# Kernel tuning notes

Hardware: AMD Instinct MI355X
Metric: run time of the kernel (lower is better)

The kernel has to match this reference:

```python
import jax, jax.numpy as jnp
import numpy as np

W = 64          # word_embedding_size
ES = 64         # entity_embedding_size
H = 4           # head_num
DH = W // H
K = 3           # convolution_num
NW, NQ, NE, NR = 50000, 20000, 200000, 100000
LQ, LR, EP, B = 8, 16, 500000, 1024
D = ES + W      # propagated entity feature dim


def _mhsa_mean(x, Wq, bq, Wk, bk, Wv, bv, Wo, bo):
    # x: [N, L, W] -> [N, W]; standard multi-head self-attention then mean over L
    N, L, _ = x.shape
    q = (x @ Wq + bq).reshape(N, L, H, DH)
    k = (x @ Wk + bk).reshape(N, L, H, DH)
    v = (x @ Wv + bv).reshape(N, L, H, DH)
    s = jnp.einsum('nlhd,nmhd->nhlm', q, k) / jnp.sqrt(jnp.asarray(DH, x.dtype))
    a = jax.nn.softmax(s, axis=-1)
    o = jnp.einsum('nhlm,nmhd->nlhd', a, v).reshape(N, L, W)
    return (o @ Wo + bo).mean(axis=1)


def setup_inputs() -> dict:
    key = jax.random.key(0)
    ks = jax.random.split(key, 20)
    f = jnp.float32
    inp = {
        'word_emb': jax.random.normal(ks[0], (NW, W), f) * 0.02,
        'entity_emb': jax.random.normal(ks[1], (NE, ES), f) * 0.02,
        'Wq': jax.random.normal(ks[2], (W, W), f) * (1.0 / np.sqrt(W)),
        'bq': jnp.zeros((W,), f),
        'Wk': jax.random.normal(ks[3], (W, W), f) * (1.0 / np.sqrt(W)),
        'bk': jnp.zeros((W,), f),
        'Wv': jax.random.normal(ks[4], (W, W), f) * (1.0 / np.sqrt(W)),
        'bv': jnp.zeros((W,), f),
        'Wo': jax.random.normal(ks[5], (W, W), f) * (1.0 / np.sqrt(W)),
        'bo': jnp.zeros((W,), f),
        'review_words': jax.random.randint(ks[6], (NR, LR), 0, NW),
        'query_words_graph': jax.random.randint(ks[7], (NQ, LQ), 0, NW),
        'profile_dst': jax.random.randint(ks[8], (NR,), 0, NE),
        'pur_src': jax.random.randint(ks[9], (EP,), 0, NE),
        'pur_dst': jax.random.randint(ks[10], (EP,), 0, NE),
        'pur_qid': jax.random.randint(ks[11], (EP,), 0, NQ),
        'users': jax.random.randint(ks[12], (B,), 0, NE),
        'items': jax.random.randint(ks[13], (B,), 0, NE),
        'negs': jax.random.randint(ks[14], (B,), 0, NE),
        'query_words': jax.random.randint(ks[15], (B, LQ), 0, NW),
    }
    return inp


def reference(word_emb, entity_emb, Wq, bq, Wk, bk, Wv, bv, Wo, bo,
              review_words, query_words_graph, profile_dst,
              pur_src, pur_dst, pur_qid, users, items, negs, query_words):
    seg = jax.ops.segment_sum
    attn = lambda x: _mhsa_mean(x, Wq, bq, Wk, bk, Wv, bv, Wo, bo)
    we = word_emb.at[0].set(0.0)  # padding_idx=0

    # composes: word -> review / query (mailbox attention reduce)
    rev_h = attn(we[review_words])              # [NR, W]
    q_h = attn(we[query_words_graph])           # [NQ, W]
    q_e0 = jnp.concatenate([jnp.zeros((NQ, ES), we.dtype), q_h], axis=-1)  # [NQ, D]

    # profiles: review -> entity, mean by in-degree
    deg_p = jnp.clip(seg(jnp.ones((NR,), we.dtype), profile_dst, num_segments=NE), 1.0)[:, None]
    prof = seg(rev_h, profile_dst, num_segments=NE) / deg_p   # [NE, W]
    e = jnp.concatenate([entity_emb, prof], axis=-1)          # e_0: [NE, D]

    # deg_i = out_deg(purchased) + out_deg(purchased_by), clamped
    ones_e = jnp.ones((EP,), we.dtype)
    deg_i = jnp.clip(seg(ones_e, pur_src, num_segments=NE)
                     + seg(ones_e, pur_dst, num_segments=NE), 1.0)[:, None]
    inv = 1.0 / jnp.sqrt(deg_i)                               # [NE, 1]

    es = [e]
    for _ in range(K):
        msg = e * inv                                         # e_k / sqrt(deg_i)
        m_pur = e[pur_src] + q_e0[pur_qid] * inv[pur_src]     # msg_u_i UDF
        nxt = seg(m_pur, pur_dst, num_segments=NE) \
            + seg(msg[pur_dst], pur_src, num_segments=NE)     # purchased_by (reverse)
        e = nxt * inv
        es.append(e)
    efin = sum(es) / (K + 1)                                  # [NE, D]

    # batch scoring
    u = efin[users]
    qb = attn(we[query_words])                                # [B, W]
    p = u + jnp.concatenate([jnp.zeros((B, ES), we.dtype), qb], axis=-1)
    pos = jnp.sum(p * efin[items], axis=-1)
    neg = jnp.sum(p * efin[negs], axis=-1)
    loss = -jnp.mean(jax.nn.log_sigmoid(pos - neg))           # BPR loss
    return loss
```

## Files before the change

kernel.cpp:

```cpp
#include <hip/hip_runtime.h>
#include <hip/hip_fp8.h>
#include <cstdint>

#define CDIV(a,b) (((a)+(b)-1)/(b))

typedef __attribute__((ext_vector_type(8))) short bf16x8;
typedef __attribute__((ext_vector_type(4))) float f32x4;
typedef __attribute__((ext_vector_type(8))) float f32x8;
typedef __attribute__((ext_vector_type(4))) _Float16 half4;
typedef __attribute__((ext_vector_type(8))) _Float16 half8;

#define QK_SCALE 32.0f
#define SCORE_SCALE (0.25f / (QK_SCALE * QK_SCALE))
#define EXP2_C (SCORE_SCALE * 1.44269504089f)

#define ES_SCALE 64.0f

__device__ __forceinline__ float bf2f(short s) {
    return __builtin_bit_cast(float, ((unsigned)(unsigned short)s) << 16);
}
__device__ __forceinline__ short rtne(float f) {
    const unsigned u = __builtin_bit_cast(unsigned, f);
    return (short)((u + 0x7fffu + ((u >> 16) & 1u)) >> 16);
}
__device__ __forceinline__ unsigned pack2r(float lo, float hi) {
    return (unsigned)(unsigned short)rtne(lo) | ((unsigned)(unsigned short)rtne(hi) << 16);
}
__device__ __forceinline__ float fp8tof(unsigned char b) {
    __hip_fp8_e4m3 t; t.__x = b; return (float)t;
}
__device__ __forceinline__ unsigned char ftofp8(float f) {
    __hip_fp8_e4m3 t(f); return t.__x;
}
__device__ __forceinline__ f32x8 fp8x8tof32(long v) {
    union { long l; unsigned char b[8]; } u; u.l = v;
    f32x8 r;
    #pragma unroll
    for (int j = 0; j < 8; ++j) r[j] = fp8tof(u.b[j]);
    return r;
}
__device__ __forceinline__ long f32x8tofp8(f32x8 a) {
    union { long l; unsigned char b[8]; } u;
    #pragma unroll
    for (int j = 0; j < 8; ++j) u.b[j] = ftofp8(a[j]);
    return u.l;
}

template<int CTRL>
__device__ __forceinline__ float dpp_add(float x) {
    const int t = __builtin_amdgcn_update_dpp(0, __builtin_bit_cast(int, x),
                                              CTRL, 0xf, 0xf, true);
    return x + __builtin_bit_cast(float, t);
}
__device__ __forceinline__ float rowsum16(float x) {
    x = dpp_add<0x108>(x);
    x = dpp_add<0x104>(x);
    x = dpp_add<0x102>(x);
    x = dpp_add<0x101>(x);
    return x;
}


__device__ __forceinline__ void prep_body(int bid,
    const float* __restrict__ we, const short* __restrict__ Wt,
    const float* __restrict__ bq, const float* __restrict__ bk,
    const float* __restrict__ bv, unsigned char* __restrict__ WQKV, int NW)
{
    const int wave = threadIdx.x >> 6;
    const int lane = threadIdx.x & 63;
    const int quad = lane >> 4;
    const int lm   = lane & 15;
    const int ntiles = CDIV(NW, 16);

    bf16x8 bfr[3][4][2];
    #pragma unroll
    for (int p = 0; p < 3; ++p)
        #pragma unroll
        for (int nt = 0; nt < 4; ++nt)
            #pragma unroll
            for (int kh = 0; kh < 2; ++kh)
                bfr[p][nt][kh] = *(const bf16x8*)(Wt + ((p*64 + nt*16 + lm)*64) + kh*32 + quad*8);
    float bias[3][4];
    #pragma unroll
    for (int nt = 0; nt < 4; ++nt) {
        bias[0][nt] = bq[nt*16 + lm];
        bias[1][nt] = bk[nt*16 + lm];
        bias[2][nt] = bv[nt*16 + lm];
    }

    #pragma unroll
    for (int t = 0; t < 4; ++t) {
        const int tile = (bid*4 + wave)*4 + t;
        if (tile >= ntiles) return;
        const int wb = tile*16;
        int w = wb + lm;
        if (w >= NW) w = NW - 1;
        const float* xr = we + (size_t)w*64;
        union { unsigned u[4]; bf16x8 v; } a0, a1;
        const float4 f0 = *(const float4*)(xr + quad*8);
        const float4 f1 = *(const float4*)(xr + quad*8 + 4);
        const float4 f2 = *(const float4*)(xr + 32 + quad*8);
        const float4 f3 = *(const float4*)(xr + 32 + quad*8 + 4);
        a0.u[0] = pack2r(f0.x, f0.y); a0.u[1] = pack2r(f0.z, f0.w);
        a0.u[2] = pack2r(f1.x, f1.y); a0.u[3] = pack2r(f1.z, f1.w);
        a1.u[0] = pack2r(f2.x, f2.y); a1.u[1] = pack2r(f2.z, f2.w);
        a1.u[2] = pack2r(f3.x, f3.y); a1.u[3] = pack2r(f3.z, f3.w);
        if (w == 0) {
            a0.u[0]=0u; a0.u[1]=0u; a0.u[2]=0u; a0.u[3]=0u;
            a1.u[0]=0u; a1.u[1]=0u; a1.u[2]=0u; a1.u[3]=0u;
        }
        #pragma unroll
        for (int p = 0; p < 3; ++p) {
            #pragma unroll
            for (int nt = 0; nt < 4; ++nt) {
                f32x4 c = {bias[p][nt], bias[p][nt], bias[p][nt], bias[p][nt]};
                c = __builtin_amdgcn_mfma_f32_16x16x32_bf16(a0.v, bfr[p][nt][0], c, 0, 0, 0);
                c = __builtin_amdgcn_mfma_f32_16x16x32_bf16(a1.v, bfr[p][nt][1], c, 0, 0, 0);
                #pragma unroll
                for (int r = 0; r < 4; ++r) {
                    const int w2 = wb + quad*4 + r;
                    if (w2 < NW) {
                        unsigned char* rowo = WQKV + (size_t)w2*192;
                        const int base = (p == 2) ? 128 : (p == 0) ? 64 : 0;
                        rowo[base + nt*16 + lm] = ftofp8(c[r] * QK_SCALE);
                    }
                }
            }
        }
    }
}

__device__ __forceinline__ void fill_body(int bid,
    const int* __restrict__ src, const int* __restrict__ dst,
    const int* __restrict__ qid,
    int* __restrict__ curC, int2* __restrict__ cmb2, int EP)
{
    const int t = bid*256 + threadIdx.x;
    if (t >= EP) return;
    const int s = src[t], d = dst[t];
    const int p1 = atomicAdd(&curC[d], 1);
    int2 e1; e1.x = s; e1.y = qid[t];
    cmb2[p1] = e1;
    const int p2 = atomicAdd(&curC[s], 1);
    int2 e2; e2.x = d | (int)0x80000000; e2.y = 0;
    cmb2[p2] = e2;
}

__device__ __forceinline__ void mark_body(int bid,
    const int* __restrict__ users, const int* __restrict__ items,
    const int* __restrict__ negs, int B, unsigned* __restrict__ lev,
    int* __restrict__ listS, int* __restrict__ list2, int* __restrict__ list1,
    int* __restrict__ nS, int* __restrict__ n2, int* __restrict__ n1)
{
    const int t = bid*256 + threadIdx.x;
    if (t >= 3*B) return;
    const int which = t / B, b = t - which*B;
    const int v = (which == 0) ? users[b] : (which == 1) ? items[b] : negs[b];
    const unsigned old = atomicMax(&lev[v], 3u);
    if (old < 3u) {
        listS[atomicAdd(nS, 1)] = v;
        list2[atomicAdd(n2, 1)] = v;
        list1[atomicAdd(n1, 1)] = v;
    }
}

__device__ __forceinline__ void expand_body(int bid, int nb, unsigned targ,
    const int* __restrict__ slist, const int* __restrict__ pn,
    const int* __restrict__ offC, const int* __restrict__ endC,
    const int2* __restrict__ cmb2, unsigned* __restrict__ lev,
    int* __restrict__ dl1, int* __restrict__ dn1,
    int* __restrict__ dl2, int* __restrict__ dn2)
{
    const int n = *pn;
    const int stride = nb * 256;
    for (int t = bid*256 + threadIdx.x; t < n; t += stride) {
        const int v = slist[t];
        const int b0 = offC[v], e0 = endC[v];
        for (int i = b0; i < e0; ++i) {
            const int u = cmb2[i].x & 0x7fffffff;
            const unsigned old = atomicMax(&lev[u], targ);
            if (old < targ) {
                dl1[atomicAdd(dn1, 1)] = u;
                if (dl2) dl2[atomicAdd(dn2, 1)] = u;
            }
        }
    }
}

__device__ __forceinline__ void finalize_body(int bid,
    const float* __restrict__ emb, const float* __restrict__ prof,
    unsigned char* __restrict__ e8, float* __restrict__ inv,
    const unsigned* __restrict__ deg_p, const unsigned* __restrict__ cntC, int NE)
{
    const int t = bid*256 + threadIdx.x;
    const int v = t >> 5;
    if (v >= NE) return;
    const int c = (t & 31) * 4;
    float4 ev;
    if (c < 64) {
        ev = *(const float4*)&emb[(size_t)v*64 + c];
    } else {
        ev = *(const float4*)&prof[(size_t)v*64 + (c - 64)];
        const unsigned dp = deg_p[v];
        const float r = 1.0f / (float)(dp > 1u ? dp : 1u);
        ev.x *= r; ev.y *= r; ev.z *= r; ev.w *= r;
    }
    union { unsigned u; unsigned char b[4]; } pk;
    pk.b[0] = ftofp8(ev.x * ES_SCALE);
    pk.b[1] = ftofp8(ev.y * ES_SCALE);
    pk.b[2] = ftofp8(ev.z * ES_SCALE);
    pk.b[3] = ftofp8(ev.w * ES_SCALE);
    *(unsigned*)&e8[(size_t)v*128 + c] = pk.u;
    if (c == 0) {
        const unsigned di = cntC[v];
        inv[v] = 1.0f / sqrtf((float)(di > 1u ? di : 1u));
    }
}

__device__ __forceinline__ void qconst_body(int bid, int nb,
    const _Float16* __restrict__ q_h16, const float* __restrict__ inv,
    const int* __restrict__ offC, const int* __restrict__ endC,
    const int2* __restrict__ cmb2,
    const int* __restrict__ list, const int* __restrict__ pn,
    _Float16* __restrict__ qc)
{
    const int n = *pn;
    const int stride = nb * 256;
    for (int t = bid*256 + threadIdx.x; (t >> 3) < n; t += stride) {
        const int v = list[t >> 3];
        const int c = (t & 7) * 8;
        f32x8 a = {0.f,0.f,0.f,0.f,0.f,0.f,0.f,0.f};
        const int b0 = offC[v], e0 = endC[v];
        for (int i = b0; i < e0; ++i) {
            const int2 e = cmb2[i];
            if (e.x >= 0) {
                const float invs = inv[e.x];
                const half8 qh = *(const half8*)&q_h16[(size_t)e.y*64 + c];
                a += __builtin_convertvector(qh, f32x8) * invs;
            }
        }
        a *= ES_SCALE;
        *(half8*)&qc[(size_t)v*64 + c] = __builtin_convertvector(a, half8);
    }
}

__device__ __forceinline__ void gather_body(int bid,
    const unsigned char* __restrict__ e8, const int* __restrict__ users,
    const int* __restrict__ items, const int* __restrict__ negs,
    float* __restrict__ acc, int B)
{
    const int t = bid*256 + threadIdx.x;
    const int r = t >> 4;
    if (r >= 3*B) return;
    const int c = (t & 15) * 8;
    const int which = r / B, b = r - which*B;
    const int idx = (which == 0) ? users[b] : (which == 1) ? items[b] : negs[b];
    const long ev = *(const long*)&e8[(size_t)idx*128 + c];
    f32x8 a = *(const f32x8*)&acc[(size_t)r*128 + c];
    a += fp8x8tof32(ev);
    *(f32x8*)&acc[(size_t)r*128 + c] = a;
}

__device__ __forceinline__ void prop_list_body(int bid, int nb,
    const unsigned char* __restrict__ e_cur, const _Float16* __restrict__ qc,
    const float* __restrict__ inv,
    const int* __restrict__ offC, const int* __restrict__ endC,
    const int2* __restrict__ cmb2,
    const int* __restrict__ list, const int* __restrict__ pn,
    unsigned char* __restrict__ e_nxt)
{
    const int n = *pn;
    const int stride = nb * 256;
    for (int t = bid*256 + threadIdx.x; (t >> 4) < n; t += stride) {
        const int v = list[t >> 4];
        const int c = (t & 15) * 8;
        f32x8 a = {0.f,0.f,0.f,0.f,0.f,0.f,0.f,0.f};
        if (c >= 64) {
            const half8 q = *(const half8*)&qc[(size_t)v*64 + (c - 64)];
            a = __builtin_convertvector(q, f32x8);
        }
        const int b0 = offC[v], e0 = endC[v];
        int un = (b0 < e0) ? cmb2[b0].x : 0;
        for (int i = b0; i < e0; ++i) {
            const int uc = un;
            if (i + 1 < e0) un = cmb2[i + 1].x;
            const int u = uc & 0x7fffffff;
            const long es = *(const long*)&e_cur[(size_t)u*128 + c];
            const float w = (uc < 0) ? inv[u] : 1.0f;
            a += fp8x8tof32(es) * w;
        }
        a *= inv[v];
        *(long*)&e_nxt[(size_t)v*128 + c] = f32x8tofp8(a);
    }
}

struct TileRegs { int4 v0; long qf[4], kf[4]; };

__device__ __forceinline__ void load_tile(
    const unsigned char* __restrict__ WQKV, int w, int quad, TileRegs& t)
{
    const unsigned char* row = WQKV + (size_t)w * 192;
    t.v0 = *(const int4*)(row + 128 + quad*16);
    #pragma unroll
    for (int h = 0; h < 4; ++h) {
        if (quad < 2) {
            t.kf[h] = *(const long*)(row +      h*16 + quad*8);
            t.qf[h] = *(const long*)(row + 64 + h*16 + quad*8);
        } else {
            t.kf[h] = 0; t.qf[h] = 0;
        }
    }
}

template<int L, int MODE>
__device__ __forceinline__ void attn_body(
    unsigned char* __restrict__ smem,
    const unsigned char* __restrict__ WQKV, const int* __restrict__ words,
    const short* __restrict__ WoT, const float* __restrict__ bo,
    int N, void* __restrict__ outp, const int* __restrict__ sidx, int bid)
{
    constexpr int SPT = 16 / L;
    constexpr int SB  = 16 * SPT;
    unsigned char (*v_s)[16*80] = (unsigned char (*)[16*80])smem;
    float (*pbar_s)[64]         = (float (*)[64])(smem + 5120);
    float (*mo_s)[68]           = (float (*)[68])(smem + 6144);

    const int wave = threadIdx.x >> 6;
    const int lane = threadIdx.x & 63;
    const int quad = lane >> 4;
    const int lm   = lane & 15;
    const int tok_total = N * L;
    const float invL = 1.0f / ((float)L * QK_SCALE);

    int wid[4];
    #pragma unroll
    for (int t = 0; t < 4; ++t) {
        int tg = (bid*16 + wave*4 + t)*16 + lm;
        if (tg >= tok_total) tg = tok_total - 1;
        wid[t] = words[tg];
    }

    TileRegs cur, nxt;
    load_tile(WQKV, wid[0], quad, cur);

    #pragma unroll
    for (int ti = 0; ti < 4; ++ti) {
        if (ti < 3) load_tile(WQKV, wid[ti+1], quad, nxt);

        *(int4*)&v_s[wave][lm*80 + quad*16] = cur.v0;

        const bool mvalid = (SPT == 1) ? true : ((quad >> 1) == ((lm >> 3) & 1));

        #pragma unroll
        for (int h = 0; h < 4; ++h) {
            const f32x4 s4 = __builtin_amdgcn_mfma_f32_16x16x32_fp8_fp8(
                cur.kf[h], cur.qf[h], (f32x4){0.f,0.f,0.f,0.f}, 0, 0, 0);
            float sv0 = s4[0], sv1 = s4[1], sv2 = s4[2], sv3 = s4[3];
            if (!mvalid) { sv0 = sv1 = sv2 = sv3 = -3.0e38f; }
            float p0 = __builtin_amdgcn_exp2f(sv0*EXP2_C),
                  p1 = __builtin_amdgcn_exp2f(sv1*EXP2_C),
                  p2 = __builtin_amdgcn_exp2f(sv2*EXP2_C),
                  p3 = __builtin_amdgcn_exp2f(sv3*EXP2_C);
            float sm = p0+p1+p2+p3;
            sm += __shfl_xor(sm, 16, 64);
            sm += __shfl_xor(sm, 32, 64);
            const float rinv = __builtin_amdgcn_rcpf(sm);
            p0 *= rinv; p1 *= rinv; p2 *= rinv; p3 *= rinv;
            p0 = rowsum16(p0); p1 = rowsum16(p1);
            p2 = rowsum16(p2); p3 = rowsum16(p3);
            if (lm == 0) {
                pbar_s[wave][h*16 + quad*4 + 0] = p0 * invL;
                pbar_s[wave][h*16 + quad*4 + 1] = p1 * invL;
                pbar_s[wave][h*16 + quad*4 + 2] = p2 * invL;
                pbar_s[wave][h*16 + quad*4 + 3] = p3 * invL;
            }
        }

        #pragma unroll
        for (int s = 0; s < SPT; ++s) {
            f32x4 pb[4];
            #pragma unroll
            for (int j = 0; j < 4; ++j)
                pb[j] = *(const f32x4*)&pbar_s[wave][quad*16 + j*4];
            float o = 0.f;
            #pragma unroll
            for (int j2 = 0; j2 < L; ++j2) {
                const int m = s*L + j2;
                o += pb[m >> 2][m & 3] * fp8tof(v_s[wave][m*80 + lane]);
            }
            mo_s[(wave*4+ti)*SPT + s][lane] = o;
        }

        if (ti < 3) {
            cur.v0 = nxt.v0;
            #pragma unroll
            for (int h = 0; h < 4; ++h) { cur.qf[h] = nxt.qf[h]; cur.kf[h] = nxt.kf[h]; }
        }
    }
    __syncthreads();

    const int col = wave*16 + lm;
    const short* bT = WoT + col*64;
    const bf16x8 b0 = *(const bf16x8*)(bT + quad*8);
    const bf16x8 b1 = *(const bf16x8*)(bT + 32 + quad*8);
    const float boc = bo[col];
    #pragma unroll
    for (int rt = 0; rt < SPT; ++rt) {
        const float* ar = mo_s[rt*16 + lm];
        const float4 fA0 = *(const float4*)(ar + quad*8);
        const float4 fA1 = *(const float4*)(ar + quad*8 + 4);
        const float4 fA2 = *(const float4*)(ar + 32 + quad*8);
        const float4 fA3 = *(const float4*)(ar + 32 + quad*8 + 4);
        union { unsigned u[4]; bf16x8 v; } a0, a1;
        a0.u[0] = pack2r(fA0.x, fA0.y); a0.u[1] = pack2r(fA0.z, fA0.w);
        a0.u[2] = pack2r(fA1.x, fA1.y); a0.u[3] = pack2r(fA1.z, fA1.w);
        a1.u[0] = pack2r(fA2.x, fA2.y); a1.u[1] = pack2r(fA2.z, fA2.w);
        a1.u[2] = pack2r(fA3.x, fA3.y); a1.u[3] = pack2r(fA3.z, fA3.w);
        f32x4 c = {boc, boc, boc, boc};
        c = __builtin_amdgcn_mfma_f32_16x16x32_bf16(a0.v, b0, c, 0, 0, 0);
        c = __builtin_amdgcn_mfma_f32_16x16x32_bf16(a1.v, b1, c, 0, 0, 0);
        #pragma unroll
        for (int r = 0; r < 4; ++r) {
            const int seq = bid*SB + rt*16 + quad*4 + r;
            if (seq < N) {
                if (MODE == 0)
                    ((float*)outp)[(size_t)seq*64 + col] = c[r];
                else if (MODE == 1)
                    atomicAdd(&((float*)outp)[(size_t)sidx[seq]*64 + col], c[r]);
                else
                    ((_Float16*)outp)[(size_t)seq*64 + col] = (_Float16)c[r];
            }
        }
    }
}


__global__ __launch_bounds__(256) void mega_build(
    const int* __restrict__ src, const int* __restrict__ dst,
    const int* __restrict__ qid, int* __restrict__ curC,
    int2* __restrict__ cmb2, int EP, int nbF,
    const float* __restrict__ we, const short* __restrict__ Wt,
    const float* __restrict__ bq, const float* __restrict__ bk,
    const float* __restrict__ bv, unsigned char* __restrict__ WQKV, int NW, int nbP,
    const int* __restrict__ users, const int* __restrict__ items,
    const int* __restrict__ negs, int B, unsigned* __restrict__ lev,
    int* __restrict__ listS, int* __restrict__ list2, int* __restrict__ list1,
    int* __restrict__ nS, int* __restrict__ n2, int* __restrict__ n1)
{
    const int b = blockIdx.x;
    if (b < nbF)            fill_body(b, src, dst, qid, curC, cmb2, EP);
    else if (b < nbF + nbP) prep_body(b - nbF, we, Wt, bq, bk, bv, WQKV, NW);
    else                    mark_body(b - nbF - nbP, users, items, negs, B, lev,
                                      listS, list2, list1, nS, n2, n1);
}

__global__ __launch_bounds__(256) void mega_attn(
    const unsigned char* __restrict__ WQKV,
    const int* __restrict__ listS, const int* __restrict__ nS,
    const int* __restrict__ offC, const int* __restrict__ endC,
    const int2* __restrict__ cmb2, unsigned* __restrict__ lev,
    int* __restrict__ list2, int* __restrict__ n2,
    int* __restrict__ list1, int* __restrict__ n1,
    const int* __restrict__ w1, int N1, float* __restrict__ o1,
    const int* __restrict__ sidx1, int nb1,
    const int* __restrict__ w2, int N2, _Float16* __restrict__ o2, int nb2,
    const int* __restrict__ w3, int N3, float* __restrict__ o3,
    const short* __restrict__ WoT, const float* __restrict__ bo)
{
    __shared__ __align__(16) unsigned char smem[6144 + 32*68*4];
    const int b = blockIdx.x;
    if (b < 64) {
        expand_body(b, 64, 2u, listS, nS, offC, endC, cmb2, lev,
                    list2, n2, list1, n1);
        return;
    }
    const int ba = b - 64;
    if (ba < nb1)
        attn_body<16,1>(smem, WQKV, w1, WoT, bo, N1, o1, sidx1, ba);
    else if (ba < nb1 + nb2)
        attn_body<8,2>(smem, WQKV, w2, WoT, bo, N2, o2, nullptr, ba - nb1);
    else
        attn_body<8,0>(smem, WQKV, w3, WoT, bo, N3, o3, nullptr, ba - nb1 - nb2);
}

__global__ __launch_bounds__(256) void mega_final(
    const int* __restrict__ list2, const int* __restrict__ n2,
    const int* __restrict__ offC, const int* __restrict__ endC,
    const int2* __restrict__ cmb2, unsigned* __restrict__ lev,
    int* __restrict__ list1, int* __restrict__ n1,
    const float* __restrict__ emb, const float* __restrict__ prof,
    unsigned char* __restrict__ e8, float* __restrict__ inv,
    const unsigned* __restrict__ deg_p, const unsigned* __restrict__ cntC, int NE)
{
    const int b = blockIdx.x;
    if (b < 256)
        expand_body(b, 256, 1u, list2, n2, offC, endC, cmb2, lev,
                    list1, n1, nullptr, nullptr);
    else
        finalize_body(b - 256, emb, prof, e8, inv, deg_p, cntC, NE);
}

__global__ __launch_bounds__(256) void mega_qg(
    const _Float16* __restrict__ q_h16, const float* __restrict__ inv,
    const int* __restrict__ offC, const int* __restrict__ endC,
    const int2* __restrict__ cmb2,
    const int* __restrict__ list1, const int* __restrict__ n1,
    _Float16* __restrict__ qc,
    const unsigned char* __restrict__ e8, const int* __restrict__ users,
    const int* __restrict__ items, const int* __restrict__ negs,
    float* __restrict__ acc, int B)
{
    const int b = blockIdx.x;
    if (b < 512) qconst_body(b, 512, q_h16, inv, offC, endC, cmb2, list1, n1, qc);
    else         gather_body(b - 512, e8, users, items, negs, acc, B);
}

__global__ __launch_bounds__(256) void mega_pg(
    const unsigned char* __restrict__ e_cur, const _Float16* __restrict__ qc,
    const float* __restrict__ inv,
    const int* __restrict__ offC, const int* __restrict__ endC,
    const int2* __restrict__ cmb2,
    const int* __restrict__ list2, const int* __restrict__ n2,
    unsigned char* __restrict__ e_nxt,
    const int* __restrict__ users, const int* __restrict__ items,
    const int* __restrict__ negs, float* __restrict__ acc, int B)
{
    const int b = blockIdx.x;
    if (b < 512) prop_list_body(b, 512, e_cur, qc, inv, offC, endC, cmb2,
                                list2, n2, e_nxt);
    else         gather_body(b - 512, e_cur, users, items, negs, acc, B);
}


__global__ __launch_bounds__(256) void misc_kernel(
    const int* __restrict__ src, const int* __restrict__ dst,
    unsigned* __restrict__ cntC, int EP,
    const int* __restrict__ pdst, unsigned* __restrict__ deg_p, int NR,
    const float* __restrict__ Wo, short* __restrict__ WoT,
    const float* __restrict__ Wq, const float* __restrict__ Wk,
    const float* __restrict__ Wv, short* __restrict__ Wt)
{
    const int t = blockIdx.x*256 + threadIdx.x;
    if (t < EP) {
        const int s = src[t], d = dst[t];
        atomicAdd(&cntC[d], 1u); atomicAdd(&cntC[s], 1u);
    }
    if (t < NR) atomicAdd(&deg_p[pdst[t]], 1u);
    if (t < 4096) {
        const int j = t >> 6, k = t & 63;
        WoT[j*64 + k] = rtne(Wo[k*64 + j]);
    }
    if (t < 3*4096) {
        const int p = t >> 12, n = (t >> 6) & 63, k = t & 63;
        const float* W = (p==0) ? Wq : (p==1) ? Wk : Wv;
        Wt[t] = rtne(W[k*64 + n]);
    }
}

#define SCAN_CHUNK 2048

__global__ __launch_bounds__(256) void scan_reduce_kernel(
    const unsigned* __restrict__ cnt, unsigned* __restrict__ part, int n)
{
    const int b = blockIdx.x;
    const int base = b * SCAN_CHUNK;
    unsigned s = 0;
    #pragma unroll
    for (int i = 0; i < 8; ++i) {
        const int idx = base + i*256 + threadIdx.x;
        if (idx < n) s += cnt[idx];
    }
    #pragma unroll
    for (int off = 1; off < 64; off <<= 1) s += __shfl_xor(s, off, 64);
    __shared__ unsigned wsum[4];
    if ((threadIdx.x & 63) == 0) wsum[threadIdx.x >> 6] = s;
    __syncthreads();
    if (threadIdx.x == 0) part[b] = wsum[0]+wsum[1]+wsum[2]+wsum[3];
}

__global__ __launch_bounds__(1024) void scan_part_kernel(
    unsigned* __restrict__ part, int NB)
{
    __shared__ unsigned a[1024];
    const int t = threadIdx.x;
    a[t] = (t < NB) ? part[t] : 0u;
    __syncthreads();
    for (int d = 1; d < 1024; d <<= 1) {
        const unsigned xa = (t >= d) ? a[t-d] : 0u;
        __syncthreads();
        a[t] += xa;
        __syncthreads();
    }
    if (t < NB) part[t] = (t > 0) ? a[t-1] : 0u;
}

__global__ __launch_bounds__(256) void scan_final_kernel(
    const unsigned* __restrict__ cnt, const unsigned* __restrict__ part,
    int* __restrict__ off, int* __restrict__ cur, int n)
{
    const int b = blockIdx.x;
    __shared__ unsigned v[SCAN_CHUNK];
    __shared__ unsigned tsum[256];
    const int base = b * SCAN_CHUNK;
    const int t = threadIdx.x;
    #pragma unroll
    for (int i = 0; i < 8; ++i) {
        const int idx = base + i*256 + t;
        v[i*256 + t] = (idx < n) ? cnt[idx] : 0u;
    }
    __syncthreads();
    unsigned s = 0;
    #pragma unroll
    for (int i = 0; i < 8; ++i) s += v[t*8 + i];
    tsum[t] = s;
    __syncthreads();
    for (int d = 1; d < 256; d <<= 1) {
        const unsigned x = (t >= d) ? tsum[t-d] : 0u;
        __syncthreads();
        tsum[t] += x;
        __syncthreads();
    }
    unsigned run = ((t > 0) ? tsum[t-1] : 0u) + part[b];
    #pragma unroll
    for (int i = 0; i < 8; ++i) {
        const int idx = base + t*8 + i;
        if (idx < n) { off[idx] = (int)run; cur[idx] = (int)run; run += v[t*8+i]; }
    }
}

__global__ __launch_bounds__(256) void prop_list_kernel(
    const unsigned char* __restrict__ e_cur, const _Float16* __restrict__ qc,
    const float* __restrict__ inv,
    const int* __restrict__ offC, const int* __restrict__ endC,
    const int2* __restrict__ cmb2,
    const int* __restrict__ list, const int* __restrict__ pn,
    unsigned char* __restrict__ e_nxt)
{
    prop_list_body(blockIdx.x, gridDim.x, e_cur, qc, inv, offC, endC, cmb2,
                   list, pn, e_nxt);
}

__global__ __launch_bounds__(256) void prop_batch_kernel(
    const unsigned char* __restrict__ e_cur, const _Float16* __restrict__ qc,
    const float* __restrict__ inv,
    const int* __restrict__ offC, const int* __restrict__ endC,
    const int2* __restrict__ cmb2,
    const int* __restrict__ users, const int* __restrict__ items,
    const int* __restrict__ negs, float* __restrict__ acc, int B)
{
    const int t = blockIdx.x*256 + threadIdx.x;
    const int r = t >> 4;
    if (r >= 3*B) return;
    const int c = (t & 15) * 8;
    const int which = r / B, b = r - which*B;
    const int v = (which == 0) ? users[b] : (which == 1) ? items[b] : negs[b];
    f32x8 a = {0.f,0.f,0.f,0.f,0.f,0.f,0.f,0.f};
    if (c >= 64) {
        const half8 q = *(const half8*)&qc[(size_t)v*64 + (c - 64)];
        a = __builtin_convertvector(q, f32x8);
    }
    const int b0 = offC[v], e0 = endC[v];
    int un = (b0 < e0) ? cmb2[b0].x : 0;
    for (int i = b0; i < e0; ++i) {
        const int uc = un;
        if (i + 1 < e0) un = cmb2[i + 1].x;
        const int u = uc & 0x7fffffff;
        const long es = *(const long*)&e_cur[(size_t)u*128 + c];
        const float w = (uc < 0) ? inv[u] : 1.0f;
        a += fp8x8tof32(es) * w;
    }
    a *= inv[v];
    a += fp8x8tof32(*(const long*)&e_cur[(size_t)v*128 + c]);
    f32x8 ac = *(const f32x8*)&acc[(size_t)r*128 + c];
    ac += a;
    *(f32x8*)&acc[(size_t)r*128 + c] = ac;
}

__global__ __launch_bounds__(128) void loss_kernel(
    const float* __restrict__ acc, const float* __restrict__ qb,
    float* __restrict__ out, int B, float invB)
{
    const int b = blockIdx.x, d = threadIdx.x;
    const float u = acc[(size_t)b*128 + d] * (0.25f / ES_SCALE);
    const float p = u + (d >= 64 ? qb[(size_t)b*64 + (d - 64)] : 0.f);
    const float ei = acc[(size_t)(B + b)*128 + d];
    const float en = acc[(size_t)(2*B + b)*128 + d];
    float x = p * (ei - en) * (0.25f / ES_SCALE);
    #pragma unroll
    for (int off = 1; off < 64; off <<= 1) x += __shfl_xor(x, off, 64);
    __shared__ float wred[2];
    if ((threadIdx.x & 63) == 0) wred[threadIdx.x >> 6] = x;
    __syncthreads();
    if (threadIdx.x == 0) {
        const float xx = wred[0] + wred[1];
        const float ls = fminf(xx, 0.f) - log1pf(expf(-fabsf(xx)));
        atomicAdd(out, -ls * invB);
    }
}

extern "C" void kernel_launch(void* const* d_in, const int* in_sizes, int n_in,
                              void* d_out, int out_size, void* d_ws, size_t ws_size,
                              hipStream_t stream)
{
    const float* word_emb        = (const float*)d_in[0];
    const float* entity_emb      = (const float*)d_in[1];
    const float* Wq = (const float*)d_in[2];  const float* bq = (const float*)d_in[3];
    const float* Wk = (const float*)d_in[4];  const float* bk = (const float*)d_in[5];
    const float* Wv = (const float*)d_in[6];  const float* bv = (const float*)d_in[7];
    const float* Wo = (const float*)d_in[8];  const float* bo = (const float*)d_in[9];
    const int* review_words      = (const int*)d_in[10];
    const int* query_words_graph = (const int*)d_in[11];
    const int* profile_dst       = (const int*)d_in[12];
    const int* pur_src           = (const int*)d_in[13];
    const int* pur_dst           = (const int*)d_in[14];
    const int* pur_qid           = (const int*)d_in[15];
    const int* users             = (const int*)d_in[16];
    const int* items             = (const int*)d_in[17];
    const int* negs              = (const int*)d_in[18];
    const int* query_words       = (const int*)d_in[19];

    const int NW = in_sizes[0]  / 64;
    const int NE = in_sizes[1]  / 64;
    const int NR = in_sizes[10] / 16;
    const int NQ = in_sizes[11] / 8;
    const int EP = in_sizes[13];
    const int B  = in_sizes[16];
    const int NB = CDIV(NE, SCAN_CHUNK);

    char* ws = (char*)d_ws;
    size_t off = 0;
    auto alloc = [&](size_t bytes) -> char* {
        char* q = ws + off; off += (bytes + 255) & ~(size_t)255; return q;
    };
    float*         prof  = (float*)         alloc((size_t)NE*64*4);
    unsigned char* e8A   = (unsigned char*) alloc((size_t)NE*128);
    unsigned char* e8B   = (unsigned char*) alloc((size_t)NE*128);
    _Float16*      q_h16 = (_Float16*)      alloc((size_t)NQ*64*2);
    float*         qb    = (float*)         alloc((size_t)B*64*4);
    float*         acc   = (float*)         alloc((size_t)3*B*128*4);
    unsigned*  deg_p   = (unsigned*) alloc((size_t)NE*4);
    unsigned*  cntC    = (unsigned*) alloc((size_t)NE*4);
    unsigned*  lev     = (unsigned*) alloc((size_t)NE*4);
    int*       fcnt    = (int*)      alloc(256);
    int*       offC    = (int*)      alloc((size_t)NE*4);
    int*       curC    = (int*)      alloc((size_t)NE*4);
    int2*      cmb2    = (int2*)     alloc((size_t)2*EP*8);
    int*       listS   = (int*)      alloc((size_t)3*B*4);
    int*       list2   = (int*)      alloc((size_t)NE*4);
    int*       list1   = (int*)      alloc((size_t)NE*4);
    float*     inv     = (float*)    alloc((size_t)NE*4);
    unsigned*  part    = (unsigned*) alloc((size_t)NB*4);
    short*     WoT     = (short*)    alloc((size_t)64*64*2);
    short*     Wt      = (short*)    alloc((size_t)3*64*64*2);

    if (off > ws_size) return;

    unsigned char* WQKV = e8A;
    _Float16* qc = (_Float16*)prof;
    int* nS = fcnt; int* n2 = fcnt + 1; int* n1 = fcnt + 2;

    const size_t zlen = (size_t)((char*)fcnt - (char*)deg_p) + 256;
    hipMemsetAsync(deg_p, 0, zlen, stream);
    hipMemsetAsync(prof,  0, (size_t)NE*64*4, stream);
    hipMemsetAsync(acc,   0, (size_t)3*B*128*4, stream);
    hipMemsetAsync(d_out, 0, (size_t)out_size*4, stream);

    misc_kernel<<<CDIV(EP, 256), 256, 0, stream>>>(pur_src, pur_dst, cntC, EP,
        profile_dst, deg_p, NR, Wo, WoT, Wq, Wk, Wv, Wt);
    scan_reduce_kernel<<<NB, 256, 0, stream>>>(cntC, part, NE);
    scan_part_kernel<<<1, 1024, 0, stream>>>(part, NB);
    scan_final_kernel<<<NB, 256, 0, stream>>>(cntC, part, offC, curC, NE);

    const int nbF = CDIV(EP, 256);
    const int nbP = CDIV(CDIV(NW, 16), 16);
    const int nbM = CDIV(3*B, 256);
    mega_build<<<nbF + nbP + nbM, 256, 0, stream>>>(
        pur_src, pur_dst, pur_qid, curC, cmb2, EP, nbF,
        word_emb, Wt, bq, bk, bv, WQKV, NW, nbP,
        users, items, negs, B, lev, listS, list2, list1, nS, n2, n1);

    const int nb1 = CDIV(NR, 16), nb2 = CDIV(NQ, 32), nb3 = CDIV(B, 32);
    mega_attn<<<64 + nb1 + nb2 + nb3, 256, 0, stream>>>(WQKV,
        listS, nS, offC, curC, cmb2, lev, list2, n2, list1, n1,
        review_words, NR, prof, profile_dst, nb1,
        query_words_graph, NQ, q_h16, nb2,
        query_words, B, qb, WoT, bo);

    mega_final<<<256 + CDIV(NE*32, 256), 256, 0, stream>>>(
        list2, n2, offC, curC, cmb2, lev, list1, n1,
        entity_emb, prof, e8A, inv, deg_p, cntC, NE);

    mega_qg<<<512 + CDIV(3*B*16, 256), 256, 0, stream>>>(
        q_h16, inv, offC, curC, cmb2, list1, n1, qc,
        e8A, users, items, negs, acc, B);

    prop_list_kernel<<<2048, 256, 0, stream>>>(e8A, qc, inv,
        offC, curC, cmb2, list1, n1, e8B);

    mega_pg<<<512 + CDIV(3*B*16, 256), 256, 0, stream>>>(
        e8B, qc, inv, offC, curC, cmb2, list2, n2, e8A,
        users, items, negs, acc, B);

    prop_batch_kernel<<<CDIV(3*B*16, 256), 256, 0, stream>>>(e8A, qc, inv,
        offC, curC, cmb2, users, items, negs, acc, B);

    loss_kernel<<<B, 128, 0, stream>>>(acc, qb, (float*)d_out, B, 1.0f / (float)B);
}
```

Before: 518.8 us.

## Regroup kernel stages so projection prep overlaps scan and fill overlaps attention

Batch-node marking moves into misc_kernel. The word-embedding QKV prep is fused with the scan reduce. The CSR fill now runs inside the attention megakernel rather than a separate build kernel, and the first frontier expansion becomes its own small kernel launched after attention. The goal is to fill idle GPU time in the tiny scan phases and cut one dependency stage, at the cost of an extra launch for the expand step and atomic-heavy fill blocks competing with attention blocks.

New measurement: 525.7 us. No clear change (+1.3%).

```diff
diff --git a/kernel.cpp b/kernel.cpp
--- a/kernel.cpp
+++ b/kernel.cpp
@@ -144,24 +144,6 @@
     const int p2 = atomicAdd(&curC[s], 1);
     int2 e2; e2.x = d | (int)0x80000000; e2.y = 0;
     cmb2[p2] = e2;
-}
-
-__device__ __forceinline__ void mark_body(int bid,
-    const int* __restrict__ users, const int* __restrict__ items,
-    const int* __restrict__ negs, int B, unsigned* __restrict__ lev,
-    int* __restrict__ listS, int* __restrict__ list2, int* __restrict__ list1,
-    int* __restrict__ nS, int* __restrict__ n2, int* __restrict__ n1)
-{
-    const int t = bid*256 + threadIdx.x;
-    if (t >= 3*B) return;
-    const int which = t / B, b = t - which*B;
-    const int v = (which == 0) ? users[b] : (which == 1) ? items[b] : negs[b];
-    const unsigned old = atomicMax(&lev[v], 3u);
-    if (old < 3u) {
-        listS[atomicAdd(nS, 1)] = v;
-        list2[atomicAdd(n2, 1)] = v;
-        list1[atomicAdd(n1, 1)] = v;
-    }
 }
 
 __device__ __forceinline__ void expand_body(int bid, int nb, unsigned targ,
@@ -435,32 +417,131 @@
 }
 
 
-__global__ __launch_bounds__(256) void mega_build(
+__global__ __launch_bounds__(256) void misc_kernel(
     const int* __restrict__ src, const int* __restrict__ dst,
-    const int* __restrict__ qid, int* __restrict__ curC,
-    int2* __restrict__ cmb2, int EP, int nbF,
-    const float* __restrict__ we, const short* __restrict__ Wt,
-    const float* __restrict__ bq, const float* __restrict__ bk,
-    const float* __restrict__ bv, unsigned char* __restrict__ WQKV, int NW, int nbP,
+    unsigned* __restrict__ cntC, int EP,
+    const int* __restrict__ pdst, unsigned* __restrict__ deg_p, int NR,
+    const float* __restrict__ Wo, short* __restrict__ WoT,
+    const float* __restrict__ Wq, const float* __restrict__ Wk,
+    const float* __restrict__ Wv, short* __restrict__ Wt,
     const int* __restrict__ users, const int* __restrict__ items,
     const int* __restrict__ negs, int B, unsigned* __restrict__ lev,
     int* __restrict__ listS, int* __restrict__ list2, int* __restrict__ list1,
     int* __restrict__ nS, int* __restrict__ n2, int* __restrict__ n1)
 {
+    const int t = blockIdx.x*256 + threadIdx.x;
+    if (t < EP) {
+        const int s = src[t], d = dst[t];
+        atomicAdd(&cntC[d], 1u); atomicAdd(&cntC[s], 1u);
+    }
+    if (t < NR) atomicAdd(&deg_p[pdst[t]], 1u);
+    if (t < 4096) {
+        const int j = t >> 6, k = t & 63;
+        WoT[j*64 + k] = rtne(Wo[k*64 + j]);
+    }
+    if (t < 3*4096) {
+        const int p = t >> 12, n = (t >> 6) & 63, k = t & 63;
+        const float* W = (p==0) ? Wq : (p==1) ? Wk : Wv;
+        Wt[t] = rtne(W[k*64 + n]);
+    }
+    if (t < 3*B) {
+        const int which = t / B, b = t - which*B;
+        const int v = (which == 0) ? users[b] : (which == 1) ? items[b] : negs[b];
+        const unsigned old = atomicMax(&lev[v], 3u);
+        if (old < 3u) {
+            listS[atomicAdd(nS, 1)] = v;
+            list2[atomicAdd(n2, 1)] = v;
+            list1[atomicAdd(n1, 1)] = v;
+        }
+    }
+}
+
+#define SCAN_CHUNK 2048
+
+__device__ __forceinline__ void scan_reduce_body(int b,
+    const unsigned* __restrict__ cnt, unsigned* __restrict__ part, int n)
+{
+    const int base = b * SCAN_CHUNK;
+    unsigned s = 0;
+    #pragma unroll
+    for (int i = 0; i < 8; ++i) {
+        const int idx = base + i*256 + threadIdx.x;
+        if (idx < n) s += cnt[idx];
+    }
+    #pragma unroll
+    for (int off = 1; off < 64; off <<= 1) s += __shfl_xor(s, off, 64);
+    __shared__ unsigned wsum[4];
+    if ((threadIdx.x & 63) == 0) wsum[threadIdx.x >> 6] = s;
+    __syncthreads();
+    if (threadIdx.x == 0) part[b] = wsum[0]+wsum[1]+wsum[2]+wsum[3];
+}
+
+__global__ __launch_bounds__(256) void mega_scan_prep(
+    const unsigned* __restrict__ cnt, unsigned* __restrict__ part, int n, int NB,
+    const float* __restrict__ we, const short* __restrict__ Wt,
+    const float* __restrict__ bq, const float* __restrict__ bk,
+    const float* __restrict__ bv, unsigned char* __restrict__ WQKV, int NW)
+{
     const int b = blockIdx.x;
-    if (b < nbF)            fill_body(b, src, dst, qid, curC, cmb2, EP);
-    else if (b < nbF + nbP) prep_body(b - nbF, we, Wt, bq, bk, bv, WQKV, NW);
-    else                    mark_body(b - nbF - nbP, users, items, negs, B, lev,
-                                      listS, list2, list1, nS, n2, n1);
+    if (b < NB) scan_reduce_body(b, cnt, part, n);
+    else        prep_body(b - NB, we, Wt, bq, bk, bv, WQKV, NW);
+}
+
+__global__ __launch_bounds__(1024) void scan_part_kernel(
+    unsigned* __restrict__ part, int NB)
+{
+    __shared__ unsigned a[1024];
+    const int t = threadIdx.x;
+    a[t] = (t < NB) ? part[t] : 0u;
+    __syncthreads();
+    for (int d = 1; d < 1024; d <<= 1) {
+        const unsigned xa = (t >= d) ? a[t-d] : 0u;
+        __syncthreads();
+        a[t] += xa;
+        __syncthreads();
+    }
+    if (t < NB) part[t] = (t > 0) ? a[t-1] : 0u;
+}
+
+__global__ __launch_bounds__(256) void scan_final_kernel(
+    const unsigned* __restrict__ cnt, const unsigned* __restrict__ part,
+    int* __restrict__ off, int* __restrict__ cur, int n)
+{
+    const int b = blockIdx.x;
+    __shared__ unsigned v[SCAN_CHUNK];
+    __shared__ unsigned tsum[256];
+    const int base = b * SCAN_CHUNK;
+    const int t = threadIdx.x;
+    #pragma unroll
+    for (int i = 0; i < 8; ++i) {
+        const int idx = base + i*256 + t;
+        v[i*256 + t] = (idx < n) ? cnt[idx] : 0u;
+    }
+    __syncthreads();
+    unsigned s = 0;
+    #pragma unroll
+    for (int i = 0; i < 8; ++i) s += v[t*8 + i];
+    tsum[t] = s;
+    __syncthreads();
+    for (int d = 1; d < 256; d <<= 1) {
+        const unsigned x = (t >= d) ? tsum[t-d] : 0u;
+        __syncthreads();
+        tsum[t] += x;
+        __syncthreads();
+    }
+    unsigned run = ((t > 0) ? tsum[t-1] : 0u) + part[b];
+    #pragma unroll
+    for (int i = 0; i < 8; ++i) {
+        const int idx = base + t*8 + i;
+        if (idx < n) { off[idx] = (int)run; cur[idx] = (int)run; run += v[t*8+i]; }
+    }
 }
 
 __global__ __launch_bounds__(256) void mega_attn(
     const unsigned char* __restrict__ WQKV,
-    const int* __restrict__ listS, const int* __restrict__ nS,
-    const int* __restrict__ offC, const int* __restrict__ endC,
-    const int2* __restrict__ cmb2, unsigned* __restrict__ lev,
-    int* __restrict__ list2, int* __restrict__ n2,
-    int* __restrict__ list1, int* __restrict__ n1,
+    const int* __restrict__ src, const int* __restrict__ dst,
+    const int* __restrict__ qid, int* __restrict__ curC,
+    int2* __restrict__ cmb2, int EP, int nbF,
     const int* __restrict__ w1, int N1, float* __restrict__ o1,
     const int* __restrict__ sidx1, int nb1,
     const int* __restrict__ w2, int N2, _Float16* __restrict__ o2, int nb2,
@@ -469,18 +550,28 @@
 {
     __shared__ __align__(16) unsigned char smem[6144 + 32*68*4];
     const int b = blockIdx.x;
-    if (b < 64) {
-        expand_body(b, 64, 2u, listS, nS, offC, endC, cmb2, lev,
-                    list2, n2, list1, n1);
+    if (b < nbF) {
+        fill_body(b, src, dst, qid, curC, cmb2, EP);
         return;
     }
-    const int ba = b - 64;
+    const int ba = b - nbF;
     if (ba < nb1)
         attn_body<16,1>(smem, WQKV, w1, WoT, bo, N1, o1, sidx1, ba);
     else if (ba < nb1 + nb2)
         attn_body<8,2>(smem, WQKV, w2, WoT, bo, N2, o2, nullptr, ba - nb1);
     else
         attn_body<8,0>(smem, WQKV, w3, WoT, bo, N3, o3, nullptr, ba - nb1 - nb2);
+}
+
+__global__ __launch_bounds__(256) void expand_kernel(
+    unsigned targ, const int* __restrict__ slist, const int* __restrict__ pn,
+    const int* __restrict__ offC, const int* __restrict__ endC,
+    const int2* __restrict__ cmb2, unsigned* __restrict__ lev,
+    int* __restrict__ dl1, int* __restrict__ dn1,
+    int* __restrict__ dl2, int* __restrict__ dn2)
+{
+    expand_body(blockIdx.x, gridDim.x, targ, slist, pn, offC, endC, cmb2, lev,
+                dl1, dn1, dl2, dn2);
 }
 
 __global__ __launch_bounds__(256) void mega_final(
@@ -529,103 +620,6 @@
     if (b < 512) prop_list_body(b, 512, e_cur, qc, inv, offC, endC, cmb2,
                                 list2, n2, e_nxt);
     else         gather_body(b - 512, e_cur, users, items, negs, acc, B);
-}
-
-
-__global__ __launch_bounds__(256) void misc_kernel(
-    const int* __restrict__ src, const int* __restrict__ dst,
-    unsigned* __restrict__ cntC, int EP,
-    const int* __restrict__ pdst, unsigned* __restrict__ deg_p, int NR,
-    const float* __restrict__ Wo, short* __restrict__ WoT,
-    const float* __restrict__ Wq, const float* __restrict__ Wk,
-    const float* __restrict__ Wv, short* __restrict__ Wt)
-{
-    const int t = blockIdx.x*256 + threadIdx.x;
-    if (t < EP) {
-        const int s = src[t], d = dst[t];
-        atomicAdd(&cntC[d], 1u); atomicAdd(&cntC[s], 1u);
-    }
-    if (t < NR) atomicAdd(&deg_p[pdst[t]], 1u);
-    if (t < 4096) {
-        const int j = t >> 6, k = t & 63;
-        WoT[j*64 + k] = rtne(Wo[k*64 + j]);
-    }
-    if (t < 3*4096) {
-        const int p = t >> 12, n = (t >> 6) & 63, k = t & 63;
-        const float* W = (p==0) ? Wq : (p==1) ? Wk : Wv;
-        Wt[t] = rtne(W[k*64 + n]);
-    }
-}
-
-#define SCAN_CHUNK 2048
-
-__global__ __launch_bounds__(256) void scan_reduce_kernel(
-    const unsigned* __restrict__ cnt, unsigned* __restrict__ part, int n)
-{
-    const int b = blockIdx.x;
-    const int base = b * SCAN_CHUNK;
-    unsigned s = 0;
-    #pragma unroll
-    for (int i = 0; i < 8; ++i) {
-        const int idx = base + i*256 + threadIdx.x;
-        if (idx < n) s += cnt[idx];
-    }
-    #pragma unroll
-    for (int off = 1; off < 64; off <<= 1) s += __shfl_xor(s, off, 64);
-    __shared__ unsigned wsum[4];
-    if ((threadIdx.x & 63) == 0) wsum[threadIdx.x >> 6] = s;
-    __syncthreads();
-    if (threadIdx.x == 0) part[b] = wsum[0]+wsum[1]+wsum[2]+wsum[3];
-}
-
-__global__ __launch_bounds__(1024) void scan_part_kernel(
-    unsigned* __restrict__ part, int NB)
-{
-    __shared__ unsigned a[1024];
-    const int t = threadIdx.x;
-    a[t] = (t < NB) ? part[t] : 0u;
-    __syncthreads();
-    for (int d = 1; d < 1024; d <<= 1) {
-        const unsigned xa = (t >= d) ? a[t-d] : 0u;
-        __syncthreads();
-        a[t] += xa;
-        __syncthreads();
-    }
-    if (t < NB) part[t] = (t > 0) ? a[t-1] : 0u;
-}
-
-__global__ __launch_bounds__(256) void scan_final_kernel(
-    const unsigned* __restrict__ cnt, const unsigned* __restrict__ part,
-    int* __restrict__ off, int* __restrict__ cur, int n)
-{
-    const int b = blockIdx.x;
-    __shared__ unsigned v[SCAN_CHUNK];
-    __shared__ unsigned tsum[256];
-    const int base = b * SCAN_CHUNK;
-    const int t = threadIdx.x;
-    #pragma unroll
-    for (int i = 0; i < 8; ++i) {
-        const int idx = base + i*256 + t;
-        v[i*256 + t] = (idx < n) ? cnt[idx] : 0u;
-    }
-    __syncthreads();
-    unsigned s = 0;
-    #pragma unroll
-    for (int i = 0; i < 8; ++i) s += v[t*8 + i];
-    tsum[t] = s;
-    __syncthreads();
-    for (int d = 1; d < 256; d <<= 1) {
-        const unsigned x = (t >= d) ? tsum[t-d] : 0u;
-        __syncthreads();
-        tsum[t] += x;
-        __syncthreads();
-    }
-    unsigned run = ((t > 0) ? tsum[t-1] : 0u) + part[b];
-    #pragma unroll
-    for (int i = 0; i < 8; ++i) {
-        const int idx = base + t*8 + i;
-        if (idx < n) { off[idx] = (int)run; cur[idx] = (int)run; run += v[t*8+i]; }
-    }
 }
 
 __global__ __launch_bounds__(256) void prop_list_kernel(
@@ -766,26 +760,26 @@
     hipMemsetAsync(d_out, 0, (size_t)out_size*4, stream);
 
     misc_kernel<<<CDIV(EP, 256), 256, 0, stream>>>(pur_src, pur_dst, cntC, EP,
-        profile_dst, deg_p, NR, Wo, WoT, Wq, Wk, Wv, Wt);
-    scan_reduce_kernel<<<NB, 256, 0, stream>>>(cntC, part, NE);
+        profile_dst, deg_p, NR, Wo, WoT, Wq, Wk, Wv, Wt,
+        users, items, negs, B, lev, listS, list2, list1, nS, n2, n1);
+
+    const int nbP = CDIV(CDIV(NW, 16), 16);
+    mega_scan_prep<<<NB + nbP, 256, 0, stream>>>(cntC, part, NE, NB,
+        word_emb, Wt, bq, bk, bv, WQKV, NW);
     scan_part_kernel<<<1, 1024, 0, stream>>>(part, NB);
     scan_final_kernel<<<NB, 256, 0, stream>>>(cntC, part, offC, curC, NE);
 
     const int nbF = CDIV(EP, 256);
-    const int nbP = CDIV(CDIV(NW, 16), 16);
-    const int nbM = CDIV(3*B, 256);
-    mega_build<<<nbF + nbP + nbM, 256, 0, stream>>>(
+    const int nb1 = CDIV(NR, 16), nb2 = CDIV(NQ, 32), nb3 = CDIV(B, 32);
+    mega_attn<<<nbF + nb1 + nb2 + nb3, 256, 0, stream>>>(WQKV,
         pur_src, pur_dst, pur_qid, curC, cmb2, EP, nbF,
-        word_emb, Wt, bq, bk, bv, WQKV, NW, nbP,
-        users, items, negs, B, lev, listS, list2, list1, nS, n2, n1);
-
-    const int nb1 = CDIV(NR, 16), nb2 = CDIV(NQ, 32), nb3 = CDIV(B, 32);
-    mega_attn<<<64 + nb1 + nb2 + nb3, 256, 0, stream>>>(WQKV,
-        listS, nS, offC, curC, cmb2, lev, list2, n2, list1, n1,
         review_words, NR, prof, profile_dst, nb1,
         query_words_graph, NQ, q_h16, nb2,
         query_words, B, qb, WoT, bo);
 
+    expand_kernel<<<64, 256, 0, stream>>>(2u, listS, nS, offC, curC, cmb2, lev,
+        list2, n2, list1, n1);
+
     mega_final<<<256 + CDIV(NE*32, 256), 256, 0, stream>>>(
         list2, n2, offC, curC, cmb2, lev, list1, n1,
         entity_emb, prof, e8A, inv, deg_p, cntC, NE);
```
